# Kernel optimization log

Hardware: AMD Instinct MI355X
Metric: run time of the kernel (lower is better)

Reference implementation:

```python
import jax, jax.numpy as jnp
import numpy as np

VOCAB, EMB, WIN = 32000, 300, 5
H1, H2, NY, NZ = 300, 300, 128, 128
B, S = 32, 512


def setup_inputs() -> dict:
    key = jax.random.key(0)
    ks = jax.random.split(key, 16)
    sc = 0.05
    inp = {
        "x": jax.random.randint(ks[0], (B, S, WIN), 0, VOCAB),
        "emb": jax.random.normal(ks[1], (VOCAB, EMB), jnp.float32) * sc,
        "W_ih1": jax.random.normal(ks[2], (H1, EMB * WIN), jnp.float32) * sc,
        "W_hh1": jax.random.normal(ks[3], (H1, H1), jnp.float32) * sc,
        "b_ih1": jax.random.normal(ks[4], (H1,), jnp.float32) * sc,
        "b_hh1": jax.random.normal(ks[5], (H1,), jnp.float32) * sc,
        "W_ih2": jax.random.normal(ks[6], (H2, H1), jnp.float32) * sc,
        "W_hh2": jax.random.normal(ks[7], (H2, H2), jnp.float32) * sc,
        "b_ih2": jax.random.normal(ks[8], (H2,), jnp.float32) * sc,
        "b_hh2": jax.random.normal(ks[9], (H2,), jnp.float32) * sc,
        "fc1_w": jax.random.normal(ks[10], (NY, H1), jnp.float32) * sc,
        "fc1_b": jax.random.normal(ks[11], (NY,), jnp.float32) * sc,
        "fc2_w": jax.random.normal(ks[12], (NZ, H2), jnp.float32) * sc,
        "fc2_b": jax.random.normal(ks[13], (NZ,), jnp.float32) * sc,
    }
    return inp


def reference(x, emb, W_ih1, W_hh1, b_ih1, b_hh1, W_ih2, W_hh2, b_ih2, b_hh2,
              fc1_w, fc1_b, fc2_w, fc2_b):
    b, s, w = x.shape
    xe = emb[jnp.transpose(x, (1, 0, 2))].reshape(s, b, w * emb.shape[1])
    xe = jax.nn.relu(xe)

    h1_0 = jnp.zeros((b, W_hh1.shape[0]), xe.dtype)
    h2_0 = jnp.zeros((b, W_hh2.shape[0]), xe.dtype)

    def step(carry, xt):
        h1, h2 = carry
        h1 = jnp.tanh(xt @ W_ih1.T + b_ih1 + h1 @ W_hh1.T + b_hh1)
        h2 = jnp.tanh(h1 @ W_ih2.T + b_ih2 + h2 @ W_hh2.T + b_hh2)
        return (h1, h2), (h1, h2)

    _, (out1, out2) = jax.lax.scan(step, (h1_0, h2_0), xe)  # [S,B,H]

    out1 = jnp.transpose(out1, (1, 0, 2)).reshape(b * s, -1)
    out2 = jnp.transpose(out2, (1, 0, 2)).reshape(b * s, -1)
    out1 = out1 @ fc1_w.T + fc1_b
    out2 = out2 @ fc2_w.T + fc2_b
    return (out1, out2)
```

## Files before the change

### kernel.cpp

```cpp
#include <hip/hip_runtime.h>
#include <hip/hip_fp16.h>

#define S_LEN 512
#define BATCH 32
#define CHUNK 16

typedef _Float16 hv2  __attribute__((ext_vector_type(2)));
typedef _Float16 half8 __attribute__((ext_vector_type(8)));
typedef float    f32x4 __attribute__((ext_vector_type(4)));

__device__ __forceinline__ float dot2f(hv2 a, hv2 b, float c) {
#if __has_builtin(__builtin_amdgcn_fdot2)
    return __builtin_amdgcn_fdot2(a, b, c, false);
#else
    return c + (float)a.x * (float)b.x + (float)a.y * (float)b.y;
#endif
}

__device__ __forceinline__ float fast_tanh(float x) {
    float e = __expf(2.f * x);
    return 1.f - 2.f / (e + 1.f);
}

__device__ __forceinline__ void lds_barrier() {
    __asm__ volatile("s_waitcnt lgkmcnt(0)\n\ts_barrier" ::: "memory");
}
__device__ __forceinline__ void vm_drain() {
    __asm__ volatile("s_waitcnt vmcnt(0)" ::: "memory");
}

#define E8   1280000
#define W18  64000
#define W28  12800
#define FF8  5120
#define PREP_TOTAL8 (E8 + W18 + W28 + FF8 + FF8)

__global__ __launch_bounds__(256) void k_prep(
    const float* __restrict__ emb,  const float* __restrict__ Wih1,
    const float* __restrict__ Wih2, const float* __restrict__ fc1w,
    const float* __restrict__ fc2w,
    _Float16* __restrict__ embf, _Float16* __restrict__ Wf1,
    _Float16* __restrict__ Wf2,  _Float16* __restrict__ F1,
    _Float16* __restrict__ F2,   unsigned int* __restrict__ flags)
{
    int gid = blockIdx.x * 256 + threadIdx.x;
    if (gid < 64) flags[gid] = 0u;
    if (gid >= PREP_TOTAL8) return;

    half8 v;
    _Float16* dst;

    if (gid < E8) {
        int row = gid / 40, c8 = (gid - row * 40) * 8;
        #pragma unroll
        for (int j = 0; j < 8; ++j) {
            int c = c8 + j;
            float f = (c < 300) ? emb[(size_t)row * 300 + c] : 0.f;
            v[j] = (_Float16)(f > 0.f ? f : 0.f);
        }
        dst = embf + (size_t)gid * 8;
    } else if (gid < E8 + W18) {
        int i = gid - E8;
        int row = i / 200, c8 = (i - row * 200) * 8;
        #pragma unroll
        for (int j = 0; j < 8; ++j) {
            int c = c8 + j, w = c / 320, cc = c - w * 320;
            float f = (row < 300 && cc < 300) ? Wih1[(size_t)row * 1500 + w * 300 + cc] : 0.f;
            v[j] = (_Float16)f;
        }
        dst = Wf1 + (size_t)i * 8;
    } else if (gid < E8 + W18 + W28) {
        int i = gid - E8 - W18;
        int row = i / 40, c8 = (i - row * 40) * 8;
        #pragma unroll
        for (int j = 0; j < 8; ++j) {
            int c = c8 + j;
            float f = (row < 300 && c < 300) ? Wih2[(size_t)row * 300 + c] : 0.f;
            v[j] = (_Float16)f;
        }
        dst = Wf2 + (size_t)i * 8;
    } else if (gid < E8 + W18 + W28 + FF8) {
        int i = gid - E8 - W18 - W28;
        int row = i / 40, c8 = (i - row * 40) * 8;
        #pragma unroll
        for (int j = 0; j < 8; ++j) {
            int c = c8 + j;
            v[j] = (_Float16)((c < 300) ? fc1w[(size_t)row * 300 + c] : 0.f);
        }
        dst = F1 + (size_t)i * 8;
    } else {
        int i = gid - E8 - W18 - W28 - FF8;
        int row = i / 40, c8 = (i - row * 40) * 8;
        #pragma unroll
        for (int j = 0; j < 8; ++j) {
            int c = c8 + j;
            v[j] = (_Float16)((c < 300) ? fc2w[(size_t)row * 300 + c] : 0.f);
        }
        dst = F2 + (size_t)i * 8;
    }
    *(half8*)dst = v;
}

__global__ __launch_bounds__(256) void k_fc_mfma(
    const _Float16* __restrict__ H1, const _Float16* __restrict__ H2,
    const _Float16* __restrict__ F1, const _Float16* __restrict__ F2,
    const float* __restrict__ fb1, const float* __restrict__ fb2,
    float* __restrict__ out1, float* __restrict__ out2)
{
    const int layer = blockIdx.y;
    const _Float16* H = layer ? H2 : H1;
    const _Float16* F = layer ? F2 : F1;
    const float* bias = layer ? fb2 : fb1;
    float* out        = layer ? out2 : out1;

    const int wid  = threadIdx.x >> 6;
    const int lane = threadIdx.x & 63;
    const int m    = lane & 15;
    const int q    = lane >> 4;
    const int r0   = blockIdx.x * 128 + wid * 32;

    f32x4 acc[2][8];
    #pragma unroll
    for (int i = 0; i < 2; ++i)
        #pragma unroll
        for (int j = 0; j < 8; ++j)
            acc[i][j] = (f32x4){0.f, 0.f, 0.f, 0.f};

    const _Float16* ha = H + (size_t)(r0 + m) * 320;
    const _Float16* hb = H + (size_t)(r0 + 16 + m) * 320;

    #pragma unroll
    for (int c = 0; c < 10; ++c) {
        const int k = c * 32 + q * 8;
        half8 a0 = *(const half8*)(ha + k);
        half8 a1 = *(const half8*)(hb + k);
        #pragma unroll
        for (int nt = 0; nt < 8; ++nt) {
            half8 bf = *(const half8*)(F + (size_t)(nt * 16 + m) * 320 + k);
            acc[0][nt] = __builtin_amdgcn_mfma_f32_16x16x32_f16(a0, bf, acc[0][nt], 0, 0, 0);
            acc[1][nt] = __builtin_amdgcn_mfma_f32_16x16x32_f16(a1, bf, acc[1][nt], 0, 0, 0);
        }
    }

    #pragma unroll
    for (int nt = 0; nt < 8; ++nt) {
        const int n = nt * 16 + m;
        const float bv = bias[n];
        #pragma unroll
        for (int mt = 0; mt < 2; ++mt) {
            #pragma unroll
            for (int reg = 0; reg < 4; ++reg) {
                const int r = r0 + mt * 16 + q * 4 + reg;
                const int oidx = ((r & 31) * S_LEN + (r >> 5)) * 128 + n;
                out[oidx] = acc[mt][nt][reg] + bv;
            }
        }
    }
}

#define LDS_BYTES 52096
#define NREC 64
#define NGEMM 128

__device__ __forceinline__ void load_u_regs(float* up, const float* __restrict__ U1,
                                            int b, int t0) {
    #pragma unroll
    for (int j = 0; j < 10; ++j) {
        int e = threadIdx.x + 512 * j;
        int row = e / 300, col = e - row * 300;
        up[j] = (e < 4800) ? U1[((size_t)((t0 + row) * BATCH + b)) * 300 + col] : 0.f;
    }
}

__device__ __forceinline__ void wait_gemm(unsigned int* flags, int c) {
    if (threadIdx.x == 0) {
        while (__hip_atomic_load(&flags[32 + c], __ATOMIC_ACQUIRE,
                                 __HIP_MEMORY_SCOPE_AGENT) < 4u)
            __builtin_amdgcn_s_sleep(2);
    }
    __syncthreads();
}

__global__ __launch_bounds__(512) void k_rec_fused(
    const int* __restrict__ x, const _Float16* __restrict__ embf,
    const _Float16* __restrict__ Wf1,
    const float* __restrict__ bih1, const float* __restrict__ bhh1,
    float* __restrict__ U1, const float* __restrict__ Whh1,
    const _Float16* __restrict__ Wf2, const float* __restrict__ Whh2,
    const float* __restrict__ bih2, const float* __restrict__ bhh2,
    _Float16* __restrict__ H1f, _Float16* __restrict__ H2f,
    unsigned int* __restrict__ flags)
{
    const int tid  = threadIdx.x;

    if (blockIdx.x >= NREC) {
        const int gi   = blockIdx.x - NREC;
        const int cch  = gi >> 2;
        const int sub  = gi & 3;
        const int wid  = tid >> 6;
        const int lane = tid & 63;
        const int m    = lane & 15;
        const int q    = lane >> 4;
        const int r0   = cch * 512 + (sub >> 1) * 256 + wid * 32;
        const int n0   = (sub & 1) * 160;

        f32x4 acc[2][10];
        #pragma unroll
        for (int i = 0; i < 2; ++i)
            #pragma unroll
            for (int j = 0; j < 10; ++j)
                acc[i][j] = (f32x4){0.f, 0.f, 0.f, 0.f};

        const int rA = r0 + m, rB = r0 + 16 + m;
        const int xbA = ((rA & 31) * S_LEN + (rA >> 5)) * 5;
        const int xbB = ((rB & 31) * S_LEN + (rB >> 5)) * 5;

        for (int w = 0; w < 5; ++w) {
            const int idxA = x[xbA + w];
            const int idxB = x[xbB + w];
            const _Float16* ea = embf + (size_t)idxA * 320;
            const _Float16* eb = embf + (size_t)idxB * 320;
            const _Float16* wb = Wf1 + (size_t)w * 320;
            #pragma unroll
            for (int c = 0; c < 10; ++c) {
                const int k = c * 32 + q * 8;
                half8 a0 = *(const half8*)(ea + k);
                half8 a1 = *(const half8*)(eb + k);
                #pragma unroll
                for (int nt = 0; nt < 10; ++nt) {
                    half8 bf = *(const half8*)(wb + (size_t)(n0 + nt * 16 + m) * 1600 + k);
                    acc[0][nt] = __builtin_amdgcn_mfma_f32_16x16x32_f16(a0, bf, acc[0][nt], 0, 0, 0);
                    acc[1][nt] = __builtin_amdgcn_mfma_f32_16x16x32_f16(a1, bf, acc[1][nt], 0, 0, 0);
                }
            }
        }

        #pragma unroll
        for (int nt = 0; nt < 10; ++nt) {
            const int n = n0 + nt * 16 + m;
            if (n >= 300) continue;
            const float bias = bih1[n] + bhh1[n];
            #pragma unroll
            for (int mt = 0; mt < 2; ++mt) {
                const int rbase = r0 + mt * 16 + q * 4;
                #pragma unroll
                for (int reg = 0; reg < 4; ++reg)
                    U1[(size_t)(rbase + reg) * 300 + n] = acc[mt][nt][reg] + bias;
            }
        }
        vm_drain();
        __syncthreads();
        if (tid == 0)
            __hip_atomic_fetch_add(&flags[32 + cch], 1u,
                                   __ATOMIC_RELEASE, __HIP_MEMORY_SCOPE_AGENT);
        return;
    }

    extern __shared__ char smem[];
    float   (*partials)[304] = (float(*)[304])smem;
    _Float16 (*hc)[320]      = (_Float16(*)[320])(smem + 12160);
    float   (*uc)[304]       = (float(*)[304])(smem + 22400);
    _Float16 (*h1s)[320]     = (_Float16(*)[320])(smem + 41856);

    const bool comp = tid < 500;
    const int g    = comp ? tid / 50 : 0;
    const int rt   = comp ? tid % 50 : 0;
    const int lane = tid & 63;
    const int wid  = tid >> 6;
    const int lm   = lane & 15;
    const int lq   = lane >> 4;

    for (int i = tid; i < CHUNK * 320; i += 512)
        ((_Float16*)hc)[i] = (_Float16)0.f;

    if (blockIdx.x < 32) {
        const int b = blockIdx.x;
        hv2 w1[6][16];
        if (comp) {
            #pragma unroll
            for (int i = 0; i < 6; ++i) {
                const float* wr = Whh1 + (size_t)(rt + 50 * i) * 300 + g * 32;
                #pragma unroll
                for (int j = 0; j < 16; ++j) {
                    int c0 = g * 32 + 2 * j;
                    hv2 p;
                    p.x = (c0     < 300) ? (_Float16)wr[2 * j]     : (_Float16)0.f;
                    p.y = (c0 + 1 < 300) ? (_Float16)wr[2 * j + 1] : (_Float16)0.f;
                    w1[i][j] = p;
                }
            }
        }

        wait_gemm(flags, 0);
        float upref[10];
        load_u_regs(upref, U1, b, 0);

        for (int c = 0; c < 32; ++c) {
            const int t0 = c * CHUNK;
            if (c > 0) {
                const int tb = t0 - CHUNK;
                for (int i = tid; i < CHUNK * 40; i += 512) {
                    int row = i / 40, c8 = i - row * 40;
                    half8 v = *(const half8*)&hc[row][c8 * 8];
                    *(half8*)&H1f[((size_t)((tb + row) * BATCH + b)) * 320 + c8 * 8] = v;
                }
            }
            #pragma unroll
            for (int j = 0; j < 10; ++j) {
                int e = tid + 512 * j;
                if (e < 4800) {
                    int row = e / 300, col = e - row * 300;
                    uc[row][col] = upref[j];
                }
            }
            if (c > 0) {
                vm_drain();
                __syncthreads();
                if (tid == 0)
                    __hip_atomic_store(&flags[b], (unsigned)t0,
                                       __ATOMIC_RELEASE, __HIP_MEMORY_SCOPE_AGENT);
            }
            if (c + 1 < 32) {
                wait_gemm(flags, c + 1);
                load_u_regs(upref, U1, b, t0 + CHUNK);
            }
            lds_barrier();

            for (int s = 0; s < CHUNK; ++s) {
                if (comp) {
                    const half8* hp = (const half8*)&hc[(s - 1) & 15][g * 32];
                    float a0 = 0.f, a1 = 0.f, a2 = 0.f, a3 = 0.f, a4 = 0.f, a5 = 0.f;
                    #pragma unroll
                    for (int jj = 0; jj < 4; ++jj) {
                        half8 q8 = hp[jj];
                        const hv2* qv = (const hv2*)&q8;
                        #pragma unroll
                        for (int j4 = 0; j4 < 4; ++j4) {
                            const int j = 4 * jj + j4;
                            a0 = dot2f(w1[0][j], qv[j4], a0);
                            a1 = dot2f(w1[1][j], qv[j4], a1);
                            a2 = dot2f(w1[2][j], qv[j4], a2);
                            a3 = dot2f(w1[3][j], qv[j4], a3);
                            a4 = dot2f(w1[4][j], qv[j4], a4);
                            a5 = dot2f(w1[5][j], qv[j4], a5);
                        }
                    }
                    partials[g][rt]       = a0;
                    partials[g][rt + 50]  = a1;
                    partials[g][rt + 100] = a2;
                    partials[g][rt + 150] = a3;
                    partials[g][rt + 200] = a4;
                    partials[g][rt + 250] = a5;
                }
                lds_barrier();
                if (tid < 300) {
                    float ssum = uc[s][tid];
                    #pragma unroll
                    for (int g2 = 0; g2 < 10; ++g2)
                        ssum += partials[g2][tid];
                    hc[s][tid] = (_Float16)fast_tanh(ssum);
                }
                lds_barrier();
            }
        }
        {
            const int tb = S_LEN - CHUNK;
            for (int i = tid; i < CHUNK * 40; i += 512) {
                int row = i / 40, c8 = i - row * 40;
                half8 v = *(const half8*)&hc[row][c8 * 8];
                *(half8*)&H1f[((size_t)((tb + row) * BATCH + b)) * 320 + c8 * 8] = v;
            }
            vm_drain();
            __syncthreads();
            if (tid == 0)
                __hip_atomic_store(&flags[b], (unsigned)S_LEN,
                                   __ATOMIC_RELEASE, __HIP_MEMORY_SCOPE_AGENT);
        }
    } else {
        const int b = blockIdx.x - 32;
        hv2 whh[6][16];
        if (comp) {
            #pragma unroll
            for (int i = 0; i < 6; ++i) {
                const float* wr = Whh2 + (size_t)(rt + 50 * i) * 300 + g * 32;
                #pragma unroll
                for (int j = 0; j < 16; ++j) {
                    int c0 = g * 32 + 2 * j;
                    hv2 p;
                    p.x = (c0     < 300) ? (_Float16)wr[2 * j]     : (_Float16)0.f;
                    p.y = (c0 + 1 < 300) ? (_Float16)wr[2 * j + 1] : (_Float16)0.f;
                    whh[i][j] = p;
                }
            }
        }
        float bias = (tid < 300) ? (bih2[tid] + bhh2[tid]) : 0.f;

        for (int c = 0; c < 32; ++c) {
            const int t0 = c * CHUNK;
            if (c > 0) {
                const int tb = t0 - CHUNK;
                for (int i = tid; i < CHUNK * 40; i += 512) {
                    int row = i / 40, c8 = i - row * 40;
                    half8 v = *(const half8*)&hc[row][c8 * 8];
                    *(half8*)&H2f[((size_t)((tb + row) * BATCH + b)) * 320 + c8 * 8] = v;
                }
            }
            if (tid == 0) {
                while (__hip_atomic_load(&flags[b], __ATOMIC_ACQUIRE,
                                         __HIP_MEMORY_SCOPE_AGENT) < (unsigned)(t0 + CHUNK))
                    __builtin_amdgcn_s_sleep(2);
            }
            __syncthreads();

            for (int i = tid; i < CHUNK * 40; i += 512) {
                int row = i / 40, c8 = i - row * 40;
                *(half8*)&h1s[row][c8 * 8] =
                    *(const half8*)&H1f[((size_t)((t0 + row) * BATCH + b)) * 320 + c8 * 8];
            }
            lds_barrier();

            for (int nt = wid; nt < 19; nt += 8) {
                f32x4 acc = (f32x4){0.f, 0.f, 0.f, 0.f};
                const int n = nt * 16 + lm;
                const _Float16* wrow = Wf2 + (size_t)n * 320;
                #pragma unroll
                for (int k0 = 0; k0 < 320; k0 += 32) {
                    half8 a  = *(const half8*)&h1s[lm][k0 + lq * 8];
                    half8 bf = *(const half8*)&wrow[k0 + lq * 8];
                    acc = __builtin_amdgcn_mfma_f32_16x16x32_f16(a, bf, acc, 0, 0, 0);
                }
                #pragma unroll
                for (int reg = 0; reg < 4; ++reg)
                    uc[lq * 4 + reg][n] = acc[reg];
            }
            lds_barrier();

            for (int s = 0; s < CHUNK; ++s) {
                if (comp) {
                    const half8* hp = (const half8*)&hc[(s - 1) & 15][g * 32];
                    float a0 = 0.f, a1 = 0.f, a2 = 0.f, a3 = 0.f, a4 = 0.f, a5 = 0.f;
                    #pragma unroll
                    for (int jj = 0; jj < 4; ++jj) {
                        half8 q8 = hp[jj];
                        const hv2* qv = (const hv2*)&q8;
                        #pragma unroll
                        for (int j4 = 0; j4 < 4; ++j4) {
                            const int j = 4 * jj + j4;
                            a0 = dot2f(whh[0][j], qv[j4], a0);
                            a1 = dot2f(whh[1][j], qv[j4], a1);
                            a2 = dot2f(whh[2][j], qv[j4], a2);
                            a3 = dot2f(whh[3][j], qv[j4], a3);
                            a4 = dot2f(whh[4][j], qv[j4], a4);
                            a5 = dot2f(whh[5][j], qv[j4], a5);
                        }
                    }
                    partials[g][rt]       = a0;
                    partials[g][rt + 50]  = a1;
                    partials[g][rt + 100] = a2;
                    partials[g][rt + 150] = a3;
                    partials[g][rt + 200] = a4;
                    partials[g][rt + 250] = a5;
                }
                lds_barrier();
                if (tid < 300) {
                    float ssum = bias + uc[s][tid];
                    #pragma unroll
                    for (int g2 = 0; g2 < 10; ++g2)
                        ssum += partials[g2][tid];
                    hc[s][tid] = (_Float16)fast_tanh(ssum);
                }
                lds_barrier();
            }
        }
        {
            const int tb = S_LEN - CHUNK;
            for (int i = tid; i < CHUNK * 40; i += 512) {
                int row = i / 40, c8 = i - row * 40;
                half8 v = *(const half8*)&hc[row][c8 * 8];
                *(half8*)&H2f[((size_t)((tb + row) * BATCH + b)) * 320 + c8 * 8] = v;
            }
        }
    }
}

extern "C" void kernel_launch(void* const* d_in, const int* in_sizes, int n_in,
                              void* d_out, int out_size, void* d_ws, size_t ws_size,
                              hipStream_t stream) {
    const int*   x     = (const int*)d_in[0];
    const float* emb   = (const float*)d_in[1];
    const float* Wih1  = (const float*)d_in[2];
    const float* Whh1  = (const float*)d_in[3];
    const float* bih1  = (const float*)d_in[4];
    const float* bhh1  = (const float*)d_in[5];
    const float* Wih2  = (const float*)d_in[6];
    const float* Whh2  = (const float*)d_in[7];
    const float* bih2  = (const float*)d_in[8];
    const float* bhh2  = (const float*)d_in[9];
    const float* fc1w  = (const float*)d_in[10];
    const float* fc1b  = (const float*)d_in[11];
    const float* fc2w  = (const float*)d_in[12];
    const float* fc2b  = (const float*)d_in[13];

    float* out1 = (float*)d_out;
    float* out2 = out1 + (size_t)16384 * 128;

    char* w = (char*)d_ws;
    float*        U1    = (float*)w;
    _Float16*     H1    = (_Float16*)(w + 19660800);
    _Float16*     Wf1   = (_Float16*)(w + 30146560);
    _Float16*     Wf2   = (_Float16*)(w + 31170560);
    _Float16*     F1    = (_Float16*)(w + 31375360);
    _Float16*     F2    = (_Float16*)(w + 31457280);
    unsigned int* flags = (unsigned int*)(w + 31539200);
    _Float16*     EMBF  = (_Float16*)(w + 31539456);
    _Float16*     H2    = EMBF;

    const int prep_blocks = (PREP_TOTAL8 + 255) / 256;
    k_prep<<<prep_blocks, 256, 0, stream>>>(emb, Wih1, Wih2, fc1w, fc2w,
                                            EMBF, Wf1, Wf2, F1, F2, flags);

    k_rec_fused<<<NREC + NGEMM, 512, LDS_BYTES, stream>>>(
        x, EMBF, Wf1, bih1, bhh1, U1, Whh1, Wf2, Whh2, bih2, bhh2, H1, H2, flags);

    dim3 g(128, 2);
    k_fc_mfma<<<g, 256, 0, stream>>>(H1, H2, F1, F2, fc1b, fc2b, out1, out2);
}
```

Measured before the change: 875.4 us.

## Fuse output FC layers into recurrent kernel and throttle GEMM blocks with global counter

Removes the separate FC kernel and computes each 16-step chunk's output projection inside the recurrent blocks via MFMA directly from the LDS hidden-state tile, so layer-2 hidden states no longer go through global memory. The per-chunk GEMM completion flags are replaced by one global counter that forces in-order completion, and GEMM blocks beyond a depth of 4 chunks wait before starting. This is meant to cut a kernel launch and the H1/H2 round trips, and to limit how far the input GEMM runs ahead. In exchange, FC work now sits on the serial recurrence critical path, and the ordered counter adds spin-waiting.

```diff
diff --git a/kernel.cpp b/kernel.cpp
--- a/kernel.cpp
+++ b/kernel.cpp
@@ -28,6 +28,8 @@
 __device__ __forceinline__ void vm_drain() {
     __asm__ volatile("s_waitcnt vmcnt(0)" ::: "memory");
 }
+
+#define F_GCTR 64
 
 #define E8   1280000
 #define W18  64000
@@ -44,7 +46,7 @@
     _Float16* __restrict__ F2,   unsigned int* __restrict__ flags)
 {
     int gid = blockIdx.x * 256 + threadIdx.x;
-    if (gid < 64) flags[gid] = 0u;
+    if (gid < 128) flags[gid] = 0u;
     if (gid >= PREP_TOTAL8) return;
 
     half8 v;
@@ -101,66 +103,10 @@
     *(half8*)dst = v;
 }
 
-__global__ __launch_bounds__(256) void k_fc_mfma(
-    const _Float16* __restrict__ H1, const _Float16* __restrict__ H2,
-    const _Float16* __restrict__ F1, const _Float16* __restrict__ F2,
-    const float* __restrict__ fb1, const float* __restrict__ fb2,
-    float* __restrict__ out1, float* __restrict__ out2)
-{
-    const int layer = blockIdx.y;
-    const _Float16* H = layer ? H2 : H1;
-    const _Float16* F = layer ? F2 : F1;
-    const float* bias = layer ? fb2 : fb1;
-    float* out        = layer ? out2 : out1;
-
-    const int wid  = threadIdx.x >> 6;
-    const int lane = threadIdx.x & 63;
-    const int m    = lane & 15;
-    const int q    = lane >> 4;
-    const int r0   = blockIdx.x * 128 + wid * 32;
-
-    f32x4 acc[2][8];
-    #pragma unroll
-    for (int i = 0; i < 2; ++i)
-        #pragma unroll
-        for (int j = 0; j < 8; ++j)
-            acc[i][j] = (f32x4){0.f, 0.f, 0.f, 0.f};
-
-    const _Float16* ha = H + (size_t)(r0 + m) * 320;
-    const _Float16* hb = H + (size_t)(r0 + 16 + m) * 320;
-
-    #pragma unroll
-    for (int c = 0; c < 10; ++c) {
-        const int k = c * 32 + q * 8;
-        half8 a0 = *(const half8*)(ha + k);
-        half8 a1 = *(const half8*)(hb + k);
-        #pragma unroll
-        for (int nt = 0; nt < 8; ++nt) {
-            half8 bf = *(const half8*)(F + (size_t)(nt * 16 + m) * 320 + k);
-            acc[0][nt] = __builtin_amdgcn_mfma_f32_16x16x32_f16(a0, bf, acc[0][nt], 0, 0, 0);
-            acc[1][nt] = __builtin_amdgcn_mfma_f32_16x16x32_f16(a1, bf, acc[1][nt], 0, 0, 0);
-        }
-    }
-
-    #pragma unroll
-    for (int nt = 0; nt < 8; ++nt) {
-        const int n = nt * 16 + m;
-        const float bv = bias[n];
-        #pragma unroll
-        for (int mt = 0; mt < 2; ++mt) {
-            #pragma unroll
-            for (int reg = 0; reg < 4; ++reg) {
-                const int r = r0 + mt * 16 + q * 4 + reg;
-                const int oidx = ((r & 31) * S_LEN + (r >> 5)) * 128 + n;
-                out[oidx] = acc[mt][nt][reg] + bv;
-            }
-        }
-    }
-}
-
 #define LDS_BYTES 52096
 #define NREC 64
 #define NGEMM 128
+#define GDEPTH 4
 
 __device__ __forceinline__ void load_u_regs(float* up, const float* __restrict__ U1,
                                             int b, int t0) {
@@ -174,11 +120,33 @@
 
 __device__ __forceinline__ void wait_gemm(unsigned int* flags, int c) {
     if (threadIdx.x == 0) {
-        while (__hip_atomic_load(&flags[32 + c], __ATOMIC_ACQUIRE,
-                                 __HIP_MEMORY_SCOPE_AGENT) < 4u)
+        while (__hip_atomic_load(&flags[F_GCTR], __ATOMIC_ACQUIRE,
+                                 __HIP_MEMORY_SCOPE_AGENT) < 4u * (unsigned)(c + 1))
             __builtin_amdgcn_s_sleep(2);
     }
     __syncthreads();
+}
+
+__device__ __forceinline__ void fc_epilogue(
+    const _Float16 (*hc)[320], const _Float16* __restrict__ F,
+    const float* __restrict__ fb, float* __restrict__ out,
+    int b, int tb, int wid, int lm, int lq)
+{
+    f32x4 acc = (f32x4){0.f, 0.f, 0.f, 0.f};
+    const int n = wid * 16 + lm;
+    const _Float16* frow = F + (size_t)n * 320;
+    #pragma unroll
+    for (int k0 = 0; k0 < 320; k0 += 32) {
+        half8 a  = *(const half8*)&hc[lm][k0 + lq * 8];
+        half8 bf = *(const half8*)&frow[k0 + lq * 8];
+        acc = __builtin_amdgcn_mfma_f32_16x16x32_f16(a, bf, acc, 0, 0, 0);
+    }
+    const float bv = fb[n];
+    #pragma unroll
+    for (int reg = 0; reg < 4; ++reg) {
+        const int t = tb + lq * 4 + reg;
+        out[(size_t)(b * 512 + t) * 128 + n] = acc[reg] + bv;
+    }
 }
 
 __global__ __launch_bounds__(512) void k_rec_fused(
@@ -188,7 +156,10 @@
     float* __restrict__ U1, const float* __restrict__ Whh1,
     const _Float16* __restrict__ Wf2, const float* __restrict__ Whh2,
     const float* __restrict__ bih2, const float* __restrict__ bhh2,
-    _Float16* __restrict__ H1f, _Float16* __restrict__ H2f,
+    _Float16* __restrict__ H1f,
+    const _Float16* __restrict__ F1, const _Float16* __restrict__ F2,
+    const float* __restrict__ fb1, const float* __restrict__ fb2,
+    float* __restrict__ out1, float* __restrict__ out2,
     unsigned int* __restrict__ flags)
 {
     const int tid  = threadIdx.x;
@@ -197,6 +168,17 @@
         const int gi   = blockIdx.x - NREC;
         const int cch  = gi >> 2;
         const int sub  = gi & 3;
+
+        if (cch >= GDEPTH) {
+            if (tid == 0) {
+                while (__hip_atomic_load(&flags[F_GCTR], __ATOMIC_ACQUIRE,
+                                         __HIP_MEMORY_SCOPE_AGENT) <
+                       4u * (unsigned)(cch - GDEPTH + 1))
+                    __builtin_amdgcn_s_sleep(2);
+            }
+            __syncthreads();
+        }
+
         const int wid  = tid >> 6;
         const int lane = tid & 63;
         const int m    = lane & 15;
@@ -206,10 +188,10 @@
 
         f32x4 acc[2][10];
         #pragma unroll
-        for (int i = 0; i < 2; ++i)
+        for (int a = 0; a < 2; ++a)
             #pragma unroll
             for (int j = 0; j < 10; ++j)
-                acc[i][j] = (f32x4){0.f, 0.f, 0.f, 0.f};
+                acc[a][j] = (f32x4){0.f, 0.f, 0.f, 0.f};
 
         const int rA = r0 + m, rB = r0 + 16 + m;
         const int xbA = ((rA & 31) * S_LEN + (rA >> 5)) * 5;
@@ -250,9 +232,13 @@
         }
         vm_drain();
         __syncthreads();
-        if (tid == 0)
-            __hip_atomic_fetch_add(&flags[32 + cch], 1u,
-                                   __ATOMIC_RELEASE, __HIP_MEMORY_SCOPE_AGENT);
+        if (tid == 0) {
+            while (__hip_atomic_load(&flags[F_GCTR], __ATOMIC_ACQUIRE,
+                                     __HIP_MEMORY_SCOPE_AGENT) < 4u * (unsigned)cch)
+                __builtin_amdgcn_s_sleep(1);
+            __hip_atomic_fetch_add(&flags[F_GCTR], 1u,
+                                   __ATOMIC_ACQ_REL, __HIP_MEMORY_SCOPE_AGENT);
+        }
         return;
     }
 
@@ -304,6 +290,7 @@
                     half8 v = *(const half8*)&hc[row][c8 * 8];
                     *(half8*)&H1f[((size_t)((tb + row) * BATCH + b)) * 320 + c8 * 8] = v;
                 }
+                fc_epilogue(hc, F1, fb1, out1, b, tb, wid, lm, lq);
             }
             #pragma unroll
             for (int j = 0; j < 10; ++j) {
@@ -370,6 +357,7 @@
                 half8 v = *(const half8*)&hc[row][c8 * 8];
                 *(half8*)&H1f[((size_t)((tb + row) * BATCH + b)) * 320 + c8 * 8] = v;
             }
+            fc_epilogue(hc, F1, fb1, out1, b, tb, wid, lm, lq);
             vm_drain();
             __syncthreads();
             if (tid == 0)
@@ -398,12 +386,7 @@
         for (int c = 0; c < 32; ++c) {
             const int t0 = c * CHUNK;
             if (c > 0) {
-                const int tb = t0 - CHUNK;
-                for (int i = tid; i < CHUNK * 40; i += 512) {
-                    int row = i / 40, c8 = i - row * 40;
-                    half8 v = *(const half8*)&hc[row][c8 * 8];
-                    *(half8*)&H2f[((size_t)((tb + row) * BATCH + b)) * 320 + c8 * 8] = v;
-                }
+                fc_epilogue(hc, F2, fb2, out2, b, t0 - CHUNK, wid, lm, lq);
             }
             if (tid == 0) {
                 while (__hip_atomic_load(&flags[b], __ATOMIC_ACQUIRE,
@@ -472,14 +455,7 @@
                 lds_barrier();
             }
         }
-        {
-            const int tb = S_LEN - CHUNK;
-            for (int i = tid; i < CHUNK * 40; i += 512) {
-                int row = i / 40, c8 = i - row * 40;
-                half8 v = *(const half8*)&hc[row][c8 * 8];
-                *(half8*)&H2f[((size_t)((tb + row) * BATCH + b)) * 320 + c8 * 8] = v;
-            }
-        }
+        fc_epilogue(hc, F2, fb2, out2, b, S_LEN - CHUNK, wid, lm, lq);
     }
 }
 
@@ -505,23 +481,20 @@
     float* out2 = out1 + (size_t)16384 * 128;
 
     char* w = (char*)d_ws;
-    float*        U1    = (float*)w;
-    _Float16*     H1    = (_Float16*)(w + 19660800);
-    _Float16*     Wf1   = (_Float16*)(w + 30146560);
-    _Float16*     Wf2   = (_Float16*)(w + 31170560);
-    _Float16*     F1    = (_Float16*)(w + 31375360);
-    _Float16*     F2    = (_Float16*)(w + 31457280);
-    unsigned int* flags = (unsigned int*)(w + 31539200);
-    _Float16*     EMBF  = (_Float16*)(w + 31539456);
-    _Float16*     H2    = EMBF;
+    unsigned int* flags = (unsigned int*)w;
+    float*        U1    = (float*)(w + 512);
+    _Float16*     H1    = (_Float16*)(w + 19661312);
+    _Float16*     Wf1   = (_Float16*)(w + 30147072);
+    _Float16*     Wf2   = (_Float16*)(w + 31171072);
+    _Float16*     F1    = (_Float16*)(w + 31375872);
+    _Float16*     F2    = (_Float16*)(w + 31457792);
+    _Float16*     EMBF  = (_Float16*)(w + 31539712);
 
     const int prep_blocks = (PREP_TOTAL8 + 255) / 256;
     k_prep<<<prep_blocks, 256, 0, stream>>>(emb, Wih1, Wih2, fc1w, fc2w,
                                             EMBF, Wf1, Wf2, F1, F2, flags);
 
     k_rec_fused<<<NREC + NGEMM, 512, LDS_BYTES, stream>>>(
-        x, EMBF, Wf1, bih1, bhh1, U1, Whh1, Wf2, Whh2, bih2, bhh2, H1, H2, flags);
-
-    dim3 g(128, 2);
-    k_fc_mfma<<<g, 256, 0, stream>>>(H1, H2, F1, F2, fc1b, fc2b, out1, out2);
-}
+        x, EMBF, Wf1, bih1, bhh1, U1, Whh1, Wf2, Whh2, bih2, bhh2, H1,
+        F1, F2, fc1b, fc2b, out1, out2, flags);
+}
```

New measurement: 1.715 ms. 1.96x slower.
